# Performance work log

Measured on AMD Instinct MI355X. Metric: run time of the kernel, lower is better.

## Reference

```python
import jax, jax.numpy as jnp
import numpy as np

GAMMAS = (0.01, 0.1, 1.0, 10.0, 100.0)
FOCAL_GAMMA = 2.0
SMOOTH = 0.1
TASK_W = (0.4, 0.3, 0.3)
A_RECON, A_ORTH, A_ADV = 1.0, 0.1, 0.1
NUM_DOMAINS = 4
NUM_LABELS1 = 4


def focal_smooth(logits, targets, maskf):
    # FocalLoss.forward with smoothing > 0, masked mean
    n_classes = logits.shape[1]
    log_p = jax.nn.log_softmax(logits, axis=1)
    p = jnp.exp(log_p)
    onehot = jax.nn.one_hot(targets, n_classes, dtype=logits.dtype)
    smooth = onehot * (1.0 - SMOOTH) + SMOOTH / n_classes
    ce = -(smooth * log_p).sum(axis=1)
    pt = jnp.take_along_axis(p, targets[:, None], axis=1)[:, 0]
    loss = ce * (1.0 - pt) ** FOCAL_GAMMA
    return (loss * maskf).sum() / jnp.maximum(maskf.sum(), 1.0)


def ce_masked(logits, targets, maskf):
    log_p = jax.nn.log_softmax(logits, axis=1)
    nll = -jnp.take_along_axis(log_p, targets[:, None], axis=1)[:, 0]
    return (nll * maskf).sum() / jnp.maximum(maskf.sum(), 1.0)


def cond_mmd(feats, domains, labels, maskf):
    # Global pairwise sq-distance matrix; multi-gamma RBF kernels summed.
    sq = (feats ** 2).sum(axis=-1)                      # (B,)
    Dmat = sq[:, None] + sq[None, :] - 2.0 * feats @ feats.T  # (B,B)
    Ksum = jnp.zeros_like(Dmat)
    for g in GAMMAS:
        Ksum = Ksum + jnp.exp(-g * Dmat)
    loss = jnp.asarray(0.0, feats.dtype)
    count = jnp.asarray(0.0, feats.dtype)
    for lab in range(NUM_LABELS1):
        lm = (labels == lab).astype(feats.dtype) * maskf
        for d1 in range(NUM_DOMAINS):
            m1 = lm * (domains == d1).astype(feats.dtype)
            n1 = m1.sum()
            Km1 = Ksum @ m1
            for d2 in range(d1 + 1, NUM_DOMAINS):
                m2 = lm * (domains == d2).astype(feats.dtype)
                n2 = m2.sum()
                valid = (n1 > 1) & (n2 > 1)
                term = (m1 @ Km1) / jnp.maximum(n1, 1.0) ** 2 \
                     + (m2 @ (Ksum @ m2)) / jnp.maximum(n2, 1.0) ** 2 \
                     - 2.0 * (m2 @ Km1) / jnp.maximum(n1 * n2, 1.0)
                loss = loss + jnp.where(valid, term, 0.0)
                count = count + valid.astype(feats.dtype)
    return loss / jnp.maximum(count, 1.0)


def hsic(c, s):
    n = c.shape[0]
    c = c / jnp.maximum(jnp.linalg.norm(c, axis=-1, keepdims=True), 1e-12)
    s = s / jnp.maximum(jnp.linalg.norm(s, axis=-1, keepdims=True), 1e-12)
    K = c @ c.T
    L = s @ s.T
    Kc = K - K.mean(axis=0, keepdims=True) - K.mean(axis=1, keepdims=True) + K.mean()
    Lc = L - L.mean(axis=0, keepdims=True) - L.mean(axis=1, keepdims=True) + L.mean()
    return (Kc * Lc).sum() / (n - 1) ** 2


def setup_inputs() -> dict:
    key = jax.random.key(0)
    ks = jax.random.split(key, 20)
    B, D, H = 4096, 256, 768
    inp = {
        'logits1': jax.random.normal(ks[0], (B, 4), jnp.float32),
        'labels1': jax.random.randint(ks[1], (B,), 0, 4),
        'logits2': jax.random.normal(ks[2], (B, 6), jnp.float32),
        'labels2': jax.random.randint(ks[3], (B,), 0, 6),
        'logits3': jax.random.normal(ks[4], (B, 3), jnp.float32),
        'labels3': jax.random.randint(ks[5], (B,), 0, 3),
        'c_v': jax.random.normal(ks[6], (B, D), jnp.float32),
        's_v': jax.random.normal(ks[7], (B, D), jnp.float32),
        'c_t': jax.random.normal(ks[8], (B, D), jnp.float32),
        's_t': jax.random.normal(ks[9], (B, D), jnp.float32),
        'v_sv': jax.random.normal(ks[10], (B, NUM_DOMAINS), jnp.float32),
        'v_st': jax.random.normal(ks[11], (B, NUM_DOMAINS), jnp.float32),
        'domain_labels': jax.random.randint(ks[12], (B,), 0, NUM_DOMAINS),
        'mask': jnp.ones((B,), dtype=bool),
        'h_img_recon': jax.random.normal(ks[13], (B, H), jnp.float32),
        'h_img_orig': jax.random.normal(ks[14], (B, H), jnp.float32),
        'h_txt_recon': jax.random.normal(ks[15], (B, H), jnp.float32),
        'h_txt_orig': jax.random.normal(ks[16], (B, H), jnp.float32),
    }
    return inp


def reference(logits1, labels1, logits2, labels2, logits3, labels3,
              c_v, s_v, c_t, s_t, v_sv, v_st, domain_labels, mask,
              h_img_recon, h_img_orig, h_txt_recon, h_txt_orig):
    maskf = mask.astype(jnp.float32)
    total = jnp.asarray(0.0, jnp.float32)
    # classification (focal + label smoothing), per-task weighted
    total = total + TASK_W[0] * focal_smooth(logits1, labels1, maskf)
    total = total + TASK_W[1] * focal_smooth(logits2, labels2, maskf)
    total = total + TASK_W[2] * focal_smooth(logits3, labels3, maskf)
    # adversarial: CE on spurious domain logits + conditional MMD on causal feats
    l_adv_s = ce_masked(v_sv, domain_labels, maskf) + ce_masked(v_st, domain_labels, maskf)
    l_adv_c = cond_mmd(c_v, domain_labels, labels1, maskf) \
            + cond_mmd(c_t, domain_labels, labels1, maskf)
    total = total + A_ADV * (l_adv_s + l_adv_c)
    # orthogonality (HSIC), on unmasked features as in source
    l_orth = hsic(c_v, s_v) + hsic(c_t, s_t)
    total = total + A_ORTH * l_orth
    # reconstruction MSE
    l_recon = jnp.mean((h_img_recon - h_img_orig) ** 2) + jnp.mean((h_txt_recon - h_txt_orig) ** 2)
    total = total + A_RECON * l_recon
    return total
```

## Files before the change

### kernel.cpp

```cpp
#include <hip/hip_runtime.h>
#include <hip/hip_bf16.h>


typedef short bf16x8 __attribute__((ext_vector_type(8)));
typedef float f32x4 __attribute__((ext_vector_type(4)));
typedef unsigned long long u64;
typedef unsigned int u32;

static constexpr int D = 256;
static constexpr int H = 768;
static constexpr int NG = 16;
static constexpr float FX32 = 4294967296.f;
static constexpr float IFX32 = 2.3283064365386963e-10f;

__device__ inline void gAddFx(u64* p, float v) {
  long long q = (long long)llroundf(v * FX32);
  atomicAdd(p, (u64)q);
}
__device__ inline float fxToF(u64 v) { return (float)(long long)v * IFX32; }

__device__ inline float rbf5(float d) {
  float K = __expf(-0.01f * d);
  if (d <= 210.f) {
    K += __expf(-0.1f * d);
    if (d <= 21.f)
      K += __expf(-d) + __expf(-10.f * d) + __expf(-100.f * d);
  }
  return K;
}

__device__ inline float focal_n(const float* x, int n, int tgt,
                                float s_over_n, float oms) {
  float mx = x[0];
  for (int c = 1; c < n; ++c) mx = fmaxf(mx, x[c]);
  float se = 0.f, sx = 0.f;
  for (int c = 0; c < n; ++c) { se += __expf(x[c] - mx); sx += x[c]; }
  float logZ = mx + __logf(se);
  float ce = logZ - oms * x[tgt] - s_over_n * sx;
  float pt = __expf(x[tgt] - logZ);
  float om = 1.f - pt;
  return ce * om * om;
}

extern "C" __global__ __launch_bounds__(256) void k_pre(
    const void* __restrict__ mask, const int* __restrict__ y1,
    const int* __restrict__ dom,
    const float* __restrict__ l1, const float* __restrict__ l2,
    const float* __restrict__ l3, const int* __restrict__ y2,
    const int* __restrict__ y3,
    const float* __restrict__ vsv, const float* __restrict__ vst,
    const float* __restrict__ cv, const float* __restrict__ sv,
    const float* __restrict__ ct, const float* __restrict__ st,
    const float* __restrict__ ir, const float* __restrict__ io,
    const float* __restrict__ trc, const float* __restrict__ to,
    u64* SA, u64* GCU, u64* U64,
    int* gid, float* sq, float* inv, unsigned short* bf, u32* CNTB,
    int B, int N4, int NA, int NB) {
  __shared__ u32 sh3[3];
  __shared__ u32 cnt[17];
  __shared__ int redi[4];
  __shared__ float redf[4];
  __shared__ float redf5[5][4];
  __shared__ float ub[4][64][4];
  int bid = blockIdx.x;
  int t = threadIdx.x;

  if (bid < NA) {
    if (t < 3) sh3[t] = 0;
    if (t < 17) cnt[t] = 0;
    __syncthreads();
    u32 a = 0, b2 = 0, cd = 0;
    if (t * 16 + 15 < B) {
      uint4 wv = ((const uint4*)mask)[t];
      u32 ws[4] = {wv.x, wv.y, wv.z, wv.w};
      #pragma unroll
      for (int j = 0; j < 4; ++j) {
        a |= ws[j] & 0xffu; b2 |= ws[j] & 0xff00u; cd |= ws[j] & 0xffff0000u;
      }
    }
    if (a) atomicOr(&sh3[0], 1u);
    if (b2) atomicOr(&sh3[1], 1u);
    if (cd) atomicOr(&sh3[2], 1u);
    __syncthreads();
    int mode;
    if ((sh3[1] | sh3[2]) == 0) mode = 0;
    else if (sh3[0] == 0 && sh3[1] == 0) mode = 1;
    else mode = 2;
    int r = bid * 256 + t;
    int mi = 0;
    float s[5] = {0.f, 0.f, 0.f, 0.f, 0.f};
    if (r < B) {
      if (mode == 0)      mi = ((const int*)mask)[r] ? 1 : 0;
      else if (mode == 1) mi = (((const float*)mask)[r] != 0.f) ? 1 : 0;
      else                mi = ((const unsigned char*)mask)[r] ? 1 : 0;
      int g = -1;
      if (mi) { g = y1[r] * 4 + dom[r]; atomicAdd(&cnt[g], 1u); }
      else atomicAdd(&cnt[16], 1u);
      gid[r] = g;
      if (mi) {
        float x[6];
        for (int c = 0; c < 4; ++c) x[c] = l1[r * 4 + c];
        s[0] = focal_n(x, 4, y1[r], 0.1f / 4.f, 0.9f);
        for (int c = 0; c < 6; ++c) x[c] = l2[r * 6 + c];
        s[1] = focal_n(x, 6, y2[r], 0.1f / 6.f, 0.9f);
        for (int c = 0; c < 3; ++c) x[c] = l3[r * 3 + c];
        s[2] = focal_n(x, 3, y3[r], 0.1f / 3.f, 0.9f);
        int d = dom[r];
        for (int c = 0; c < 4; ++c) x[c] = vsv[r * 4 + c];
        {
          float mx = fmaxf(fmaxf(x[0], x[1]), fmaxf(x[2], x[3]));
          float se = __expf(x[0]-mx)+__expf(x[1]-mx)+__expf(x[2]-mx)+__expf(x[3]-mx);
          s[3] = mx + __logf(se) - x[d];
        }
        for (int c = 0; c < 4; ++c) x[c] = vst[r * 4 + c];
        {
          float mx = fmaxf(fmaxf(x[0], x[1]), fmaxf(x[2], x[3]));
          float se = __expf(x[0]-mx)+__expf(x[1]-mx)+__expf(x[2]-mx)+__expf(x[3]-mx);
          s[4] = mx + __logf(se) - x[d];
        }
      }
    }
    int v = mi;
    #pragma unroll
    for (int o = 32; o > 0; o >>= 1) {
      v += __shfl_down(v, o);
      #pragma unroll
      for (int k = 0; k < 5; ++k) s[k] += __shfl_down(s[k], o);
    }
    if ((t & 63) == 0) {
      redi[t >> 6] = v;
      #pragma unroll
      for (int k = 0; k < 5; ++k) redf5[k][t >> 6] = s[k];
    }
    __syncthreads();
    if (t == 0) {
      atomicAdd(&SA[5], (u64)(redi[0] + redi[1] + redi[2] + redi[3]));
      #pragma unroll
      for (int k = 0; k < 5; ++k)
        gAddFx(&SA[k], redf5[k][0] + redf5[k][1] + redf5[k][2] + redf5[k][3]);
    }
    if (t < NG && cnt[t]) atomicAdd(&GCU[t], (u64)cnt[t]);
    if (t < 17) CNTB[bid * 17 + t] = cnt[t];
  } else if (bid < NA + NB) {
    int b = bid - NA;
    int perF = NB >> 2;
    int f = b / perF;
    int rb = b - f * perF;
    const float* p = (f == 0) ? cv : (f == 1) ? sv : (f == 2) ? ct : st;
    int w = t >> 6, L = t & 63;
    int rbase = rb * 32 + w * 8;
    float4 vv[8];
    #pragma unroll
    for (int i = 0; i < 8; ++i)
      vv[i] = ((const float4*)(p + (size_t)(rbase + i) * D))[L];
    float ss[8];
    #pragma unroll
    for (int i = 0; i < 8; ++i)
      ss[i] = vv[i].x * vv[i].x + vv[i].y * vv[i].y
            + vv[i].z * vv[i].z + vv[i].w * vv[i].w;
    #pragma unroll
    for (int o = 32; o > 0; o >>= 1) {
      #pragma unroll
      for (int i = 0; i < 8; ++i) ss[i] += __shfl_down(ss[i], o);
    }
    #pragma unroll
    for (int i = 0; i < 8; ++i) ss[i] = __shfl(ss[i], 0);
    float up0 = 0.f, up1 = 0.f, up2 = 0.f, up3 = 0.f;
    #pragma unroll
    for (int i = 0; i < 8; ++i) {
      int r = rbase + i;
      float iv = 1.f / fmaxf(sqrtf(ss[i]), 1e-12f);
      if ((f & 1) == 0) {
        int fi = f >> 1;
        alignas(8) __hip_bfloat16 hb[4];
        hb[0] = __float2bfloat16(vv[i].x); hb[1] = __float2bfloat16(vv[i].y);
        hb[2] = __float2bfloat16(vv[i].z); hb[3] = __float2bfloat16(vv[i].w);
        *(uint2*)(bf + ((size_t)fi * B + r) * D + L * 4) = *(uint2*)hb;
        if (L == 0) sq[fi * B + r] = ss[i];
      }
      if (L == 0) inv[f * B + r] = iv;
      up0 += vv[i].x * iv; up1 += vv[i].y * iv;
      up2 += vv[i].z * iv; up3 += vv[i].w * iv;
    }
    ub[w][L][0] = up0; ub[w][L][1] = up1; ub[w][L][2] = up2; ub[w][L][3] = up3;
    __syncthreads();
    if (t < 64) {
      u64* Uf = U64 + f * D + 4 * t;
      #pragma unroll
      for (int j = 0; j < 4; ++j) {
        float s4 = ub[0][t][j] + ub[1][t][j] + ub[2][t][j] + ub[3][t][j];
        gAddFx(Uf + j, s4);
      }
    }
  } else {
    int cidx = bid - (NA + NB);
    int j = cidx >> 9;
    int cb = cidx & 511;
    const float4* A  = (const float4*)(j ? trc : ir);
    const float4* Bp = (const float4*)(j ? to : io);
    int CH = (N4 + 511) >> 9;
    int base = cb * CH;
    int end = min(base + CH, N4);
    float acc = 0.f;
    int idx = base + t;
    for (; idx + 256 < end; idx += 512) {
      float4 a0 = A[idx],       b0 = Bp[idx];
      float4 a1 = A[idx + 256], b1 = Bp[idx + 256];
      float dx0 = a0.x-b0.x, dy0 = a0.y-b0.y, dz0 = a0.z-b0.z, dw0 = a0.w-b0.w;
      float dx1 = a1.x-b1.x, dy1 = a1.y-b1.y, dz1 = a1.z-b1.z, dw1 = a1.w-b1.w;
      acc += dx0*dx0 + dy0*dy0 + dz0*dz0 + dw0*dw0
           + dx1*dx1 + dy1*dy1 + dz1*dz1 + dw1*dw1;
    }
    if (idx < end) {
      float4 a = A[idx], b = Bp[idx];
      float dx = a.x-b.x, dy = a.y-b.y, dz = a.z-b.z, dw = a.w-b.w;
      acc += dx*dx + dy*dy + dz*dz + dw*dw;
    }
    #pragma unroll
    for (int o = 32; o > 0; o >>= 1) acc += __shfl_down(acc, o);
    if ((t & 63) == 0) redf[t >> 6] = acc;
    __syncthreads();
    if (t == 0) gAddFx(&SA[6 + j], redf[0] + redf[1] + redf[2] + redf[3]);
  }
}

extern "C" __global__ __launch_bounds__(256) void k_mid(
    const u32* __restrict__ CNTB, const int* __restrict__ gid,
    const float* __restrict__ sq,
    const float* __restrict__ cv, const float* __restrict__ sv,
    const float* __restrict__ ct, const float* __restrict__ st,
    const float* __restrict__ inv,
    int* __restrict__ perm, float* __restrict__ sqp, int* __restrict__ OFF,
    unsigned short* __restrict__ bnT, int B, int NA) {
  __shared__ float ld[64 * 65];
  __shared__ u32 cbs[17], tots[17], wcnt[4][17];
  __shared__ u32 base[18];
  int b = blockIdx.x, t = threadIdx.x;

  if (b < NA) {
    if (t < 68) ((u32*)wcnt)[t] = 0;
    if (t < 17) {
      u32 cb = 0, tot = 0;
      for (int b2 = 0; b2 < NA; ++b2) {
        u32 c = CNTB[b2 * 17 + t];
        cb += (b2 < b) ? c : 0u;
        tot += c;
      }
      cbs[t] = cb; tots[t] = tot;
    }
    int r = b * 256 + t;
    int g = 16;
    if (r < B) { int gg = gid[r]; g = (gg < 0) ? 16 : gg; }
    __syncthreads();
    if (t == 0) {
      u32 s = 0;
      for (int g2 = 0; g2 < 17; ++g2) { base[g2] = s; s += tots[g2]; }
      base[17] = s;
    }
    u64 msk = ~0ull;
    #pragma unroll
    for (int bit = 0; bit < 5; ++bit) {
      int bv = (g >> bit) & 1;
      u64 bl = __ballot(bv);
      msk &= bv ? bl : ~bl;
    }
    int lane = t & 63, w = t >> 6;
    int rwave = __popcll(msk & ((1ull << lane) - 1ull));
    if (rwave == 0) wcnt[w][g] = (u32)__popcll(msk);
    __syncthreads();
    if (r < B) {
      int rank = rwave;
      for (int w2 = 0; w2 < 4; ++w2) if (w2 < w) rank += (int)wcnt[w2][g];
      int pos = (int)(base[g] + cbs[g]) + rank;
      perm[pos] = r;
      sqp[pos] = sq[r];
      sqp[B + pos] = sq[B + r];
    }
    if (b == 0 && t < 18) OFF[t] = (int)base[t];
  } else {
    int TPF = (B >> 6) * 4;
    int tb = b - NA;
    int fm = tb / TPF, tile = tb - fm * TPF;
    int it = tile >> 2, at = tile & 3;
    const float* src = (fm == 0) ? cv : (fm == 1) ? sv : (fm == 2) ? ct : st;
    const float* ivf = inv + (size_t)fm * B;
    int i0 = it * 64, a0 = at * 64;
    for (int e = t; e < 1024; e += 256) {
      int i = e >> 4, c4 = e & 15;
      float4 v = ((const float4*)(src + (size_t)(i0 + i) * D))[at * 16 + c4];
      float ivv = ivf[i0 + i];
      ld[i * 65 + c4 * 4 + 0] = v.x * ivv;
      ld[i * 65 + c4 * 4 + 1] = v.y * ivv;
      ld[i * 65 + c4 * 4 + 2] = v.z * ivv;
      ld[i * 65 + c4 * 4 + 3] = v.w * ivv;
    }
    __syncthreads();
    unsigned short* dst = bnT + (size_t)fm * D * B;
    for (int e = t; e < 512; e += 256) {
      int a = e >> 3, ic = e & 7;
      alignas(16) unsigned short h[8];
      #pragma unroll
      for (int j = 0; j < 8; ++j) {
        __hip_bfloat16 hb = __float2bfloat16(ld[(ic * 8 + j) * 65 + a]);
        h[j] = *(unsigned short*)&hb;
      }
      *(uint4*)(dst + (size_t)(a0 + a) * B + i0 + ic * 8) = *(uint4*)h;
    }
  }
}

extern "C" __global__ __launch_bounds__(256) void k_big(
    const unsigned short* __restrict__ bf, const float* __restrict__ sqp,
    const int* __restrict__ perm, const int* __restrict__ OFF,
    const unsigned short* __restrict__ bnT, float* __restrict__ Mf32,
    u64* GSP, int B) {
  __shared__ __align__(16) char smem[17536];
  unsigned short* Ab = (unsigned short*)smem;
  unsigned short* Bb = (unsigned short*)(smem + 8192);
  int bid = blockIdx.x;
  int tid = threadIdx.x;
  int w = tid >> 6, L = tid & 63, m = L & 15, q = L >> 4;
  int r0 = tid >> 3, ck = tid & 7;
  int swz = (ck ^ (r0 & 7)) * 8;
  int ar = w * 16 + m;

  if (bid < 64) {
    int half = bid & 1, bb = (bid >> 1) & 3, ab = (bid >> 3) & 3, p = (bid >> 5) & 1;
    const unsigned short* Abase = bnT + (size_t)(2 * p) * D * B;
    const unsigned short* Bbase = bnT + (size_t)(2 * p + 1) * D * B;
    size_t kof = (size_t)half * (B >> 1) + ck * 8;
    const uint4* gA0 = (const uint4*)(Abase + (size_t)(ab * 64 + r0) * B + kof);
    const uint4* gA1 = (const uint4*)(Abase + (size_t)(ab * 64 + r0 + 32) * B + kof);
    const uint4* gB0 = (const uint4*)(Bbase + (size_t)(bb * 64 + r0) * B + kof);
    const uint4* gB1 = (const uint4*)(Bbase + (size_t)(bb * 64 + r0 + 32) * B + kof);
    uint4* dA0 = (uint4*)&Ab[r0 * 64 + swz];
    uint4* dA1 = (uint4*)&Ab[(r0 + 32) * 64 + swz];
    uint4* dB0 = (uint4*)&Bb[r0 * 64 + swz];
    uint4* dB1 = (uint4*)&Bb[(r0 + 32) * 64 + swz];
    f32x4 acc[4] = {{0.f,0.f,0.f,0.f},{0.f,0.f,0.f,0.f},
                    {0.f,0.f,0.f,0.f},{0.f,0.f,0.f,0.f}};
    int nh = B >> 7;
    for (int hq = 0; hq < nh; ++hq) {
      *dA0 = gA0[hq * 8]; *dA1 = gA1[hq * 8];
      *dB0 = gB0[hq * 8]; *dB1 = gB1[hq * 8];
      __syncthreads();
      #pragma unroll
      for (int kk = 0; kk < 2; ++kk) {
        bf16x8 aF = *(const bf16x8*)&Ab[ar * 64 + (((kk * 4 + q) ^ (ar & 7)) * 8)];
        #pragma unroll
        for (int c = 0; c < 4; ++c) {
          int br = c * 16 + m;
          bf16x8 bF = *(const bf16x8*)&Bb[br * 64 + (((kk * 4 + q) ^ (br & 7)) * 8)];
          acc[c] = __builtin_amdgcn_mfma_f32_16x16x32_bf16(aF, bF, acc[c], 0, 0, 0);
        }
      }
      if (hq < nh - 1) __syncthreads();
    }
    float* Mo = Mf32 + (size_t)(half * 2 + p) * D * D;
    int ri0 = w * 16 + q * 4;
    #pragma unroll
    for (int c = 0; c < 4; ++c) {
      #pragma unroll
      for (int v = 0; v < 4; ++v)
        Mo[(size_t)(ab * 64 + ri0 + v) * D + bb * 64 + c * 16 + m] = acc[c][v];
    }
    return;
  }

  float* sA = (float*)(smem + 16384);
  float* sB = (float*)(smem + 16640);
  int*   pA = (int*)(smem + 16896);
  int*   pB = (int*)(smem + 17152);
  int*   offs = (int*)(smem + 17408);

  int idx2 = bid - 64;
  int feat = idx2 & 1;
  int tlin = idx2 >> 1;
  int NT = B / 64;
  float tf = (float)tlin;
  int ti = (int)((2.f * NT + 1.f -
                  sqrtf((2.f * NT + 1.f) * (2.f * NT + 1.f) - 8.f * tf)) * 0.5f);
  while (ti > 0 && (ti * NT - (ti * (ti - 1)) / 2) > tlin) --ti;
  while (((ti + 1) * NT - ((ti + 1) * ti) / 2) <= tlin) ++ti;
  int tj = ti + (tlin - (ti * NT - (ti * (ti - 1)) / 2));
  int i0 = ti * 64, j0 = tj * 64;
  bool diag = (ti == tj);
  const unsigned short* fb = bf + (size_t)feat * B * D;
  const float* sqf = sqp + (size_t)feat * B;

  if (tid < 64) { pA[tid] = perm[i0 + tid]; sA[tid] = sqf[i0 + tid]; }
  else if (tid < 128) { int r = tid - 64; pB[r] = perm[j0 + r]; sB[r] = sqf[j0 + r]; }
  else if (tid < 146) offs[tid - 128] = OFF[tid - 128];
  __syncthreads();

  int gr0 = 0, nbr = 0, gc0 = 0, ncb = 0;
  #pragma unroll
  for (int g = 1; g <= 17; ++g) {
    int o = offs[g];
    gr0 += (o <= i0) ? 1 : 0;
    nbr += (o > i0 && o < i0 + 64) ? 1 : 0;
    gc0 += (o <= j0) ? 1 : 0;
    ncb += (o > j0 && o < j0 + 64) ? 1 : 0;
  }
  if (gr0 == 16 || gc0 == 16) return;
  int gr1 = gr0 + nbr;
  int gc1 = gc0 + ncb;
  int s_r = nbr ? offs[gr1] : i0 + 64;
  int s_c = ncb ? offs[gc1] : j0 + 64;

  const uint4* gA0 = (const uint4*)(fb + (size_t)pA[r0] * D + ck * 8);
  const uint4* gA1 = (const uint4*)(fb + (size_t)pA[r0 + 32] * D + ck * 8);
  uint4* dA0 = (uint4*)&Ab[r0 * 64 + swz];
  uint4* dA1 = (uint4*)&Ab[(r0 + 32) * 64 + swz];
  const uint4* gB0 = nullptr; const uint4* gB1 = nullptr;
  uint4* dB0 = nullptr; uint4* dB1 = nullptr;
  if (!diag) {
    gB0 = (const uint4*)(fb + (size_t)pB[r0] * D + ck * 8);
    gB1 = (const uint4*)(fb + (size_t)pB[r0 + 32] * D + ck * 8);
    dB0 = (uint4*)&Bb[r0 * 64 + swz];
    dB1 = (uint4*)&Bb[(r0 + 32) * 64 + swz];
  }
  const unsigned short* Bp = diag ? Ab : Bb;

  f32x4 acc[4] = {{0.f,0.f,0.f,0.f},{0.f,0.f,0.f,0.f},
                  {0.f,0.f,0.f,0.f},{0.f,0.f,0.f,0.f}};

  for (int hq = 0; hq < 4; ++hq) {
    *dA0 = gA0[hq * 8]; *dA1 = gA1[hq * 8];
    if (!diag) { *dB0 = gB0[hq * 8]; *dB1 = gB1[hq * 8]; }
    __syncthreads();
    #pragma unroll
    for (int kk = 0; kk < 2; ++kk) {
      bf16x8 aF = *(const bf16x8*)&Ab[ar * 64 + (((kk * 4 + q) ^ (ar & 7)) * 8)];
      #pragma unroll
      for (int c = 0; c < 4; ++c) {
        int br = c * 16 + m;
        bf16x8 bF = *(const bf16x8*)&Bp[br * 64 + (((kk * 4 + q) ^ (br & 7)) * 8)];
        acc[c] = __builtin_amdgcn_mfma_f32_16x16x32_bf16(aF, bF, acc[c], 0, 0, 0);
      }
    }
    if (hq < 3) __syncthreads();
  }

  int ri0 = w * 16 + q * 4;
  u64* gsp = GSP + ((size_t)(tlin & 63) * 2 + feat) * NG * NG;

  if (nbr <= 1 && ncb <= 1) {
    float siv[4]; bool rhiv[4];
    #pragma unroll
    for (int v = 0; v < 4; ++v) {
      siv[v] = sA[ri0 + v];
      rhiv[v] = (i0 + ri0 + v) >= s_r;
    }
    float a00 = 0.f, a01 = 0.f, a10 = 0.f, a11 = 0.f;
    #pragma unroll
    for (int c = 0; c < 4; ++c) {
      int rj = c * 16 + m;
      float sb = sB[rj];
      float lo = 0.f, hi = 0.f;
      #pragma unroll
      for (int v = 0; v < 4; ++v) {
        float d = fmaxf(siv[v] + sb - 2.f * acc[c][v], 0.f);
        float K = rbf5(d);
        if (diag) {
          int ri = ri0 + v;
          K = (ri > rj) ? 0.f : (ri == rj) ? 5.f : K;
        }
        float kh = rhiv[v] ? K : 0.f;
        hi += kh; lo += K - kh;
      }
      bool chi = (j0 + rj) >= s_c;
      float loH = chi ? lo : 0.f;
      float hiH = chi ? hi : 0.f;
      a00 += lo - loH; a01 += loH;
      a10 += hi - hiH; a11 += hiH;
    }
    #pragma unroll
    for (int o = 32; o > 0; o >>= 1) {
      a00 += __shfl_down(a00, o); a01 += __shfl_down(a01, o);
      a10 += __shfl_down(a10, o); a11 += __shfl_down(a11, o);
    }
    if (L == 0) {
      if (a00 != 0.f)
        atomicAdd(&gsp[gr0 * NG + gc0], (u64)(long long)llroundf(a00 * 65536.f));
      if (a01 != 0.f && gc1 < 16)
        atomicAdd(&gsp[gr0 * NG + gc1], (u64)(long long)llroundf(a01 * 65536.f));
      if (a10 != 0.f && gr1 < 16)
        atomicAdd(&gsp[gr1 * NG + gc0], (u64)(long long)llroundf(a10 * 65536.f));
      if (a11 != 0.f && gr1 < 16 && gc1 < 16)
        atomicAdd(&gsp[gr1 * NG + gc1], (u64)(long long)llroundf(a11 * 65536.f));
    }
  } else {
    int giv[4]; float siv[4];
    #pragma unroll
    for (int v = 0; v < 4; ++v) {
      int idx = i0 + ri0 + v;
      int g = 0;
      #pragma unroll
      for (int k = 1; k <= 16; ++k) g += (offs[k] <= idx) ? 1 : 0;
      giv[v] = g;
      siv[v] = sA[ri0 + v];
    }
    #pragma unroll
    for (int c = 0; c < 4; ++c) {
      int rj = c * 16 + m;
      int jdx = j0 + rj;
      int gj = 0;
      #pragma unroll
      for (int k = 1; k <= 16; ++k) gj += (offs[k] <= jdx) ? 1 : 0;
      float sb = sB[rj];
      #pragma unroll
      for (int v = 0; v < 4; ++v) {
        int ri = ri0 + v;
        if (giv[v] < 16 && gj < 16 && !(diag && ri > rj)) {
          float K;
          if (diag && ri == rj) K = 5.f;
          else {
            float d = fmaxf(siv[v] + sb - 2.f * acc[c][v], 0.f);
            K = rbf5(d);
          }
          u32 kf = (u32)(K * 65536.f + 0.5f);
          atomicAdd(&gsp[giv[v] * NG + gj], (u64)kf);
        }
      }
    }
  }
}

extern "C" __global__ __launch_bounds__(256) void k_hsic(
    const u64* __restrict__ U64, const float* __restrict__ Mf32, u64* SA) {
  __shared__ float red[8];
  __shared__ float ush[32], vsh[D];
  int p = blockIdx.y;
  int k0 = blockIdx.x * 32;
  int t = threadIdx.x;
  vsh[t] = fxToF(U64[(2 * p + 1) * D + t]);
  if (t < 32) ush[t] = fxToF(U64[(2 * p) * D + k0 + t]);
  __syncthreads();
  const float* M0 = Mf32 + (size_t)p * D * D;
  const float* M1 = Mf32 + (size_t)(2 + p) * D * D;
  float trkl = 0.f, cr = 0.f;
  #pragma unroll 4
  for (int k = 0; k < 32; ++k) {
    float mv = M0[(size_t)(k0 + k) * D + t] + M1[(size_t)(k0 + k) * D + t];
    trkl += mv * mv;
    cr += ush[k] * mv;
  }
  cr *= vsh[t];
  #pragma unroll
  for (int o = 32; o > 0; o >>= 1) { trkl += __shfl_down(trkl, o); cr += __shfl_down(cr, o); }
  if ((t & 63) == 0) { red[t >> 6] = trkl; red[4 + (t >> 6)] = cr; }
  __syncthreads();
  if (t == 0) gAddFx(&SA[10 + p], red[0] + red[1] + red[2] + red[3]);
  if (t == 64) gAddFx(&SA[12 + p], red[4] + red[5] + red[6] + red[7]);
}

extern "C" __global__ __launch_bounds__(256) void k_final(
    const u64* SA, const u64* GCU, const u64* GSP,
    const u64* U64, float* out, int B) {
  __shared__ float red[8];
  __shared__ float gssh[2 * NG * NG];
  int t = threadIdx.x;
  for (int e = t; e < 2 * NG * NG; e += 256) {
    u64 ssum = 0;
    int f = e >> 8, idx = e & 255;
    for (int cpy = 0; cpy < 64; ++cpy)
      ssum += GSP[((size_t)cpy * 2 + f) * NG * NG + idx];
    gssh[e] = (float)((double)ssum * (1.0 / 65536.0));
  }
  __syncthreads();

  float n = (float)B;
  float hs[2];
  for (int p = 0; p < 2; ++p) {
    float ut = fxToF(U64[(2 * p) * D + t]);
    float vt = fxToF(U64[(2 * p + 1) * D + t]);
    float uu = ut * ut, vv = vt * vt;
    #pragma unroll
    for (int o = 32; o > 0; o >>= 1) { uu += __shfl_down(uu, o); vv += __shfl_down(vv, o); }
    __syncthreads();
    if ((t & 63) == 0) { red[t >> 6] = uu; red[4 + (t >> 6)] = vv; }
    __syncthreads();
    float uus = red[0] + red[1] + red[2] + red[3];
    float vvs = red[4] + red[5] + red[6] + red[7];
    float trkl = (float)((double)(long long)SA[10 + p] * (double)IFX32);
    float cr   = (float)((double)(long long)SA[12 + p] * (double)IFX32);
    hs[p] = (trkl - (2.f / n) * cr + uus * vvs / (n * n))
          / ((n - 1.f) * (n - 1.f));
    __syncthreads();
  }
  if (t == 0) {
    float msum = fmaxf((float)SA[5], 1.f);
    float f1 = fxToF(SA[0]) / msum;
    float f2 = fxToF(SA[1]) / msum;
    float f3 = fxToF(SA[2]) / msum;
    float cesv = fxToF(SA[3]) / msum;
    float cest = fxToF(SA[4]) / msum;
    float mmd[2];
    for (int f = 0; f < 2; ++f) {
      float loss = 0.f, cntv = 0.f;
      for (int lab = 0; lab < 4; ++lab)
        for (int d1 = 0; d1 < 4; ++d1)
          for (int d2 = d1 + 1; d2 < 4; ++d2) {
            int a = lab * 4 + d1, b = lab * 4 + d2;
            float n1 = (float)GCU[a], n2 = (float)GCU[b];
            if (n1 > 1.f && n2 > 1.f) {
              float g11 = 2.f * gssh[f * 256 + a * NG + a] - 5.f * n1;
              float g22 = 2.f * gssh[f * 256 + b * NG + b] - 5.f * n2;
              float g12 = gssh[f * 256 + a * NG + b];
              loss += g11 / (fmaxf(n1, 1.f) * fmaxf(n1, 1.f))
                    + g22 / (fmaxf(n2, 1.f) * fmaxf(n2, 1.f))
                    - 2.f * g12 / fmaxf(n1 * n2, 1.f);
              cntv += 1.f;
            }
          }
      mmd[f] = loss / fmaxf(cntv, 1.f);
    }
    double rs = ((double)(long long)SA[6] + (double)(long long)SA[7])
              * (double)IFX32;
    float recon = (float)(rs / ((double)B * (double)H));
    float total = 0.4f * f1 + 0.3f * f2 + 0.3f * f3
                + 0.1f * (cesv + cest + mmd[0] + mmd[1])
                + 0.1f * (hs[0] + hs[1])
                + recon;
    out[0] = total;
  }
}

extern "C" void kernel_launch(void* const* d_in, const int* in_sizes, int n_in,
                              void* d_out, int out_size, void* d_ws, size_t ws_size,
                              hipStream_t stream) {
  const float* l1  = (const float*)d_in[0];
  const int*   y1  = (const int*)d_in[1];
  const float* l2  = (const float*)d_in[2];
  const int*   y2  = (const int*)d_in[3];
  const float* l3  = (const float*)d_in[4];
  const int*   y3  = (const int*)d_in[5];
  const float* cv  = (const float*)d_in[6];
  const float* sv  = (const float*)d_in[7];
  const float* ct  = (const float*)d_in[8];
  const float* st  = (const float*)d_in[9];
  const float* vsv = (const float*)d_in[10];
  const float* vst = (const float*)d_in[11];
  const int*   dom = (const int*)d_in[12];
  const void*  mask= d_in[13];
  const float* ir  = (const float*)d_in[14];
  const float* io  = (const float*)d_in[15];
  const float* trc = (const float*)d_in[16];
  const float* to  = (const float*)d_in[17];
  int B = in_sizes[1];

  u64* SA  = (u64*)d_ws;
  u64* GCU = SA + 32;
  u64* U64 = GCU + 16;
  u64* GSP = U64 + 4 * D;
  u64* zend = GSP + 64 * 2 * NG * NG;
  size_t zeroBytes = (size_t)((char*)zend - (char*)d_ws);
  unsigned short* bf  = (unsigned short*)zend;
  unsigned short* bnT = bf + 2 * (size_t)B * D;
  float* Mf32 = (float*)(bnT + 4 * (size_t)D * B);
  int*   gid = (int*)(Mf32 + 4 * (size_t)D * D);
  float* sq  = (float*)(gid + B);
  float* inv = sq + 2 * B;
  int*   perm = (int*)(inv + 4 * B);
  float* sqp  = (float*)(perm + B);
  int*   OFF  = (int*)(sqp + 2 * B);
  u32*   CNTB = (u32*)(OFF + 18);

  int NA = B / 256;
  int NB = B / 8;
  int NC = 1024;
  int N4 = B * H / 4;

  hipMemsetAsync(d_ws, 0, zeroBytes, stream);
  k_pre<<<NA + NB + NC, 256, 0, stream>>>(
      mask, y1, dom, l1, l2, l3, y2, y3, vsv, vst,
      cv, sv, ct, st, ir, io, trc, to,
      SA, GCU, U64, gid, sq, inv, bf, CNTB, B, N4, NA, NB);
  int NTR = B / 4;
  k_mid<<<NA + NTR, 256, 0, stream>>>(CNTB, gid, sq, cv, sv, ct, st, inv,
                                      perm, sqp, OFF, bnT, B, NA);
  int NT = B / 64;
  int nmmd = 2 * (NT * (NT + 1) / 2);
  k_big<<<64 + nmmd, 256, 0, stream>>>(bf, sqp, perm, OFF, bnT, Mf32, GSP, B);
  k_hsic<<<dim3(8, 2), 256, 0, stream>>>(U64, Mf32, SA);
  k_final<<<1, 256, 0, stream>>>(SA, GCU, GSP, U64, (float*)d_out, B);
}
```

Measured before the change: 206.1 us.

## Merge HSIC and final kernels with flag sync; swizzle MMD tile order

Fuses the HSIC trace kernel and the final reduction kernel into one 17-block launch. Block 16 spin-waits on a global atomic counter that the 16 HSIC blocks increment after their fixed-point adds, which saves one kernel launch and its gap. It also remaps the MMD tile index in k_big so that consecutive blocks interleave across the triangular tile space, spreading load and atomic contention more evenly. The spin-wait relies on all 17 blocks being co-resident, which holds for such a small grid.

```diff
diff --git a/kernel.cpp b/kernel.cpp
--- a/kernel.cpp
+++ b/kernel.cpp
@@ -18,6 +18,15 @@
   atomicAdd(p, (u64)q);
 }
 __device__ inline float fxToF(u64 v) { return (float)(long long)v * IFX32; }
+
+__device__ inline void flagRelease(u64* f) {
+  __threadfence();
+  atomicAdd(f, 1ull);
+}
+__device__ inline void flagAcquire(u64* f, u64 n) {
+  while (atomicAdd(f, 0ull) < n) __builtin_amdgcn_s_sleep(32);
+  __threadfence();
+}
 
 __device__ inline float rbf5(float d) {
   float K = __expf(-0.01f * d);
@@ -374,9 +383,14 @@
   int*   offs = (int*)(smem + 17408);
 
   int idx2 = bid - 64;
+  int NT = B / 64;
+  {
+    int ntile = NT * (NT + 1);
+    if ((ntile & 7) == 0)
+      idx2 = (idx2 & 7) * (ntile >> 3) + (idx2 >> 3);
+  }
   int feat = idx2 & 1;
   int tlin = idx2 >> 1;
-  int NT = B / 64;
   float tf = (float)tlin;
   int ti = (int)((2.f * NT + 1.f -
                   sqrtf((2.f * NT + 1.f) * (2.f * NT + 1.f) - 8.f * tf)) * 0.5f);
@@ -527,40 +541,46 @@
   }
 }
 
-extern "C" __global__ __launch_bounds__(256) void k_hsic(
-    const u64* __restrict__ U64, const float* __restrict__ Mf32, u64* SA) {
+extern "C" __global__ __launch_bounds__(256) void k_fin(
+    const u64* __restrict__ U64, const float* __restrict__ Mf32,
+    u64* SA, const u64* __restrict__ GCU, const u64* __restrict__ GSP,
+    float* out, u64* FLG, int B) {
   __shared__ float red[8];
   __shared__ float ush[32], vsh[D];
-  int p = blockIdx.y;
-  int k0 = blockIdx.x * 32;
+  __shared__ float gssh[2 * NG * NG];
+  int bid = blockIdx.x;
   int t = threadIdx.x;
-  vsh[t] = fxToF(U64[(2 * p + 1) * D + t]);
-  if (t < 32) ush[t] = fxToF(U64[(2 * p) * D + k0 + t]);
+
+  if (bid < 16) {
+    int p = bid >> 3;
+    int k0 = (bid & 7) * 32;
+    vsh[t] = fxToF(U64[(2 * p + 1) * D + t]);
+    if (t < 32) ush[t] = fxToF(U64[(2 * p) * D + k0 + t]);
+    __syncthreads();
+    const float* M0 = Mf32 + (size_t)p * D * D;
+    const float* M1 = Mf32 + (size_t)(2 + p) * D * D;
+    float trkl = 0.f, cr = 0.f;
+    #pragma unroll 4
+    for (int k = 0; k < 32; ++k) {
+      size_t off = (size_t)(k0 + k) * D + t;
+      float mv = M0[off] + M1[off];
+      trkl += mv * mv;
+      cr += ush[k] * mv;
+    }
+    cr *= vsh[t];
+    #pragma unroll
+    for (int o = 32; o > 0; o >>= 1) { trkl += __shfl_down(trkl, o); cr += __shfl_down(cr, o); }
+    if ((t & 63) == 0) { red[t >> 6] = trkl; red[4 + (t >> 6)] = cr; }
+    __syncthreads();
+    if (t == 0) gAddFx(&SA[10 + p], red[0] + red[1] + red[2] + red[3]);
+    if (t == 64) gAddFx(&SA[12 + p], red[4] + red[5] + red[6] + red[7]);
+    __syncthreads();
+    if (t == 0) flagRelease(&FLG[0]);
+    return;
+  }
+
+  if (t == 0) flagAcquire(&FLG[0], 16ull);
   __syncthreads();
-  const float* M0 = Mf32 + (size_t)p * D * D;
-  const float* M1 = Mf32 + (size_t)(2 + p) * D * D;
-  float trkl = 0.f, cr = 0.f;
-  #pragma unroll 4
-  for (int k = 0; k < 32; ++k) {
-    float mv = M0[(size_t)(k0 + k) * D + t] + M1[(size_t)(k0 + k) * D + t];
-    trkl += mv * mv;
-    cr += ush[k] * mv;
-  }
-  cr *= vsh[t];
-  #pragma unroll
-  for (int o = 32; o > 0; o >>= 1) { trkl += __shfl_down(trkl, o); cr += __shfl_down(cr, o); }
-  if ((t & 63) == 0) { red[t >> 6] = trkl; red[4 + (t >> 6)] = cr; }
-  __syncthreads();
-  if (t == 0) gAddFx(&SA[10 + p], red[0] + red[1] + red[2] + red[3]);
-  if (t == 64) gAddFx(&SA[12 + p], red[4] + red[5] + red[6] + red[7]);
-}
-
-extern "C" __global__ __launch_bounds__(256) void k_final(
-    const u64* SA, const u64* GCU, const u64* GSP,
-    const u64* U64, float* out, int B) {
-  __shared__ float red[8];
-  __shared__ float gssh[2 * NG * NG];
-  int t = threadIdx.x;
   for (int e = t; e < 2 * NG * NG; e += 256) {
     u64 ssum = 0;
     int f = e >> 8, idx = e & 255;
@@ -654,7 +674,8 @@
   u64* GCU = SA + 32;
   u64* U64 = GCU + 16;
   u64* GSP = U64 + 4 * D;
-  u64* zend = GSP + 64 * 2 * NG * NG;
+  u64* FLG = GSP + 64 * 2 * NG * NG;
+  u64* zend = FLG + 4;
   size_t zeroBytes = (size_t)((char*)zend - (char*)d_ws);
   unsigned short* bf  = (unsigned short*)zend;
   unsigned short* bnT = bf + 2 * (size_t)B * D;
@@ -683,6 +704,5 @@
   int NT = B / 64;
   int nmmd = 2 * (NT * (NT + 1) / 2);
   k_big<<<64 + nmmd, 256, 0, stream>>>(bf, sqp, perm, OFF, bnT, Mf32, GSP, B);
-  k_hsic<<<dim3(8, 2), 256, 0, stream>>>(U64, Mf32, SA);
-  k_final<<<1, 256, 0, stream>>>(SA, GCU, GSP, U64, (float*)d_out, B);
-}
+  k_fin<<<17, 256, 0, stream>>>(U64, Mf32, SA, GCU, GSP, (float*)d_out, FLG, B);
+}
```

Measured after the change: 212.7 us. +3.2%, slower.
